# Optimization experiments

Measured on AMD Instinct MI355X. Metric: run time of the kernel, lower is better.

## Reference

```python
import jax, jax.numpy as jnp
import numpy as np

N = 20000      # total nodes (100 graphs x 200 nodes)
B = 100        # batch_size
PER = 200      # nodes per graph (uniform) -> max_num_nodes
E = 320000     # edges (before self-loops)
F_IN = 32      # num_features
HEADS = 10
OUT = 128      # output_dim
NEG_SLOPE = 0.2  # PyG GATConv default


def setup_inputs() -> dict:
    key = jax.random.key(0)
    ks = jax.random.split(key, 14)
    feats = jax.random.normal(ks[0], (N, F_IN), jnp.float32)
    src = jax.random.randint(ks[1], (E,), 0, N)
    dst = jax.random.randint(ks[2], (E,), 0, N)
    edge_index = jnp.stack([src, dst]).astype(jnp.int32)
    graph_id = jnp.repeat(jnp.arange(B, dtype=jnp.int32), PER)
    batch_num_nodes = jnp.full((B,), PER, jnp.int32)
    s1 = 1.0 / np.sqrt(F_IN)
    s2 = 1.0 / np.sqrt(F_IN * HEADS)
    s3 = 1.0 / np.sqrt(OUT)
    return {
        "feats": feats,
        "edge_index": edge_index,
        "graph_id": graph_id,
        "batch_num_nodes": batch_num_nodes,
        # GATConv 1: in F_IN -> HEADS x F_IN, concat
        "W1": jax.random.normal(ks[3], (F_IN, HEADS * F_IN), jnp.float32) * s1,
        "a1_src": jax.random.normal(ks[4], (HEADS, F_IN), jnp.float32) * s1,
        "a1_dst": jax.random.normal(ks[5], (HEADS, F_IN), jnp.float32) * s1,
        "b1": jnp.zeros((HEADS * F_IN,), jnp.float32),
        "W2": jax.random.normal(ks[6], (HEADS * F_IN, OUT), jnp.float32) * s2,
        "a2_src": jax.random.normal(ks[7], (1, OUT), jnp.float32) * s3,
        "a2_dst": jax.random.normal(ks[8], (1, OUT), jnp.float32) * s3,
        "b2": jnp.zeros((OUT,), jnp.float32),
        # shared fc_g1
        "fc_w": jax.random.normal(ks[9], (OUT, OUT), jnp.float32) * s3,
        "fc_b": jnp.zeros((OUT,), jnp.float32),
    }


def gat_conv(x, src, dst, W, a_src, a_dst, bias, heads, out_dim):
    # x: [N, Fin]; src/dst already include self-loops (PyG default add_self_loops=True)
    n = x.shape[0]
    xw = (x @ W).reshape(n, heads, out_dim)                 # [N,H,F]
    s_src = jnp.einsum('nhf,hf->nh', xw, a_src)             # [N,H]
    s_dst = jnp.einsum('nhf,hf->nh', xw, a_dst)
    e = jax.nn.leaky_relu(s_src[src] + s_dst[dst], NEG_SLOPE)  # [E,H]
    # segment softmax over incoming edges of each destination node
    m = jax.ops.segment_max(e, dst, num_segments=n)         # [N,H]
    ex = jnp.exp(e - m[dst])
    denom = jax.ops.segment_sum(ex, dst, num_segments=n)    # [N,H]
    alpha = ex / jnp.maximum(denom[dst], 1e-16)             # [E,H]
    out = jax.ops.segment_sum(alpha[:, :, None] * xw[src], dst, num_segments=n)  # [N,H,F]
    return out.reshape(n, heads * out_dim) + bias


def reference(feats, edge_index, graph_id, batch_num_nodes,
              W1, a1_src, a1_dst, b1, W2, a2_src, a2_dst, b2, fc_w, fc_b):
    n = feats.shape[0]
    loops = jnp.arange(n, dtype=edge_index.dtype)
    src = jnp.concatenate([edge_index[0], loops])
    dst = jnp.concatenate([edge_index[1], loops])
    x = feats.astype(jnp.float32)
    # dropout layers are identity in eval mode
    x = jax.nn.elu(gat_conv(x, src, dst, W1, a1_src, a1_dst, b1, HEADS, F_IN))
    x = gat_conv(x, src, dst, W2, a2_src, a2_dst, b2, 1, OUT)
    x = jax.nn.relu(x)                                       # [N, OUT]
    # dgl_split: scatter node feats into [B, max_num_nodes, OUT] padded tensor
    cum = jnp.concatenate([jnp.zeros((1,), jnp.int32),
                           jnp.cumsum(batch_num_nodes).astype(jnp.int32)])
    idx = jnp.arange(n, dtype=jnp.int32) - cum[graph_id] + graph_id * PER
    padded = jnp.zeros((B * PER, OUT), x.dtype).at[idx].set(x).reshape(B, PER, OUT)
    out = jax.nn.relu(padded @ fc_w + fc_b)                  # [B, PER, OUT]
    # global max pool per graph, then shared fc_g1 + relu
    pooled = jax.ops.segment_max(x, graph_id, num_segments=B)  # [B, OUT]
    pooled = jax.nn.relu(pooled @ fc_w + fc_b)
    return (out, pooled)
```

## Files before the change

kernel.cpp:

```cpp
#include <hip/hip_runtime.h>

#define N_NODES 20000
#define N_EDGES 320000
#define ETOT    (N_EDGES + N_NODES)
#define HEADS   10
#define F_IN    32
#define C1      (HEADS * F_IN)
#define C2      128
#define NB      100
#define PER     200
#define CAP     96
#define HSTRIDE 328
#define X2STRIDE 136

typedef __attribute__((ext_vector_type(8))) short bf16x8;
typedef __attribute__((ext_vector_type(4))) float floatx4;
typedef _Float16 f16;
typedef _Float16 f16x2 __attribute__((ext_vector_type(2)));
typedef _Float16 f16x8 __attribute__((ext_vector_type(8)));

static __device__ __forceinline__ unsigned short f2bf(float f) {
    unsigned int u = __float_as_uint(f);
    unsigned int r = (u + 0x7fffu + ((u >> 16) & 1u)) >> 16;
    return (unsigned short)r;
}

#define SCAT_BLOCKS  ((ETOT + 255) / 256)
#define SCORE_BLOCKS ((N_NODES + 63) / 64)
#define W2P_BLOCKS   ((C1 * C2 + 255) / 256)
#define W1P_BLOCKS   ((HEADS * F_IN * F_IN + 255) / 256)
#define FCP_BLOCKS   ((C2 * C2 + 255) / 256)
#define F16_BLOCKS   ((N_NODES * F_IN / 4 + 255) / 256)
__global__ __launch_bounds__(256) void mega_prep_kernel(
        const int* __restrict__ ei, int* __restrict__ cursor, int* __restrict__ csr_src,
        const float* __restrict__ feats, f16* __restrict__ feats16,
        const float* __restrict__ W1, unsigned short* __restrict__ W1p,
        const float* __restrict__ W2, unsigned short* __restrict__ W2p,
        const float* __restrict__ fcw, f16* __restrict__ FCp,
        const float* __restrict__ a1s, const float* __restrict__ a1d,
        float* __restrict__ s_src, float* __restrict__ s_dst) {
    unsigned int b = blockIdx.x;
    if (b < SCAT_BLOCKS) {
        int e = b * 256 + threadIdx.x;
        if (e >= ETOT) return;
        int s, d;
        if (e < N_EDGES) { s = ei[e]; d = ei[N_EDGES + e]; }
        else             { s = e - N_EDGES; d = s; }
        int pos = atomicAdd(&cursor[d], 1);
        csr_src[(size_t)d * CAP + pos] = s;
        return;
    }
    b -= SCAT_BLOCKS;
    if (b < SCORE_BLOCKS) {
        __shared__ __align__(16) float A[64 * F_IN];
        __shared__ float Ws[C1], Wd[C1];
        int t = threadIdx.x;
        for (int o = t; o < C1; o += 256) {
            int k = o & 31, h = o >> 5;
            float ss = 0.f, dd = 0.f;
#pragma unroll
            for (int f = 0; f < F_IN; f++) {
                float wv = W1[k * C1 + h * 32 + f];
                ss += wv * a1s[h * 32 + f];
                dd += wv * a1d[h * 32 + f];
            }
            Ws[k * HEADS + h] = ss;
            Wd[k * HEADS + h] = dd;
        }
        int n0 = b * 64;
        int nrows = min(64, N_NODES - n0);
        const float4* fs = (const float4*)(feats + (size_t)n0 * F_IN);
        float4* Af = (float4*)A;
        for (int i = t; i < nrows * 8; i += 256) Af[i] = fs[i];
        __syncthreads();
        for (int o = t; o < nrows * HEADS; o += 256) {
            int nl = o / HEADS, h = o - nl * HEADS;
            const float* ar = A + nl * F_IN;
            float ss = 0.f, dd = 0.f;
#pragma unroll
            for (int k = 0; k < F_IN; k++) {
                float av = ar[k];
                ss += av * Ws[k * HEADS + h];
                dd += av * Wd[k * HEADS + h];
            }
            s_src[(size_t)(n0 + nl) * HEADS + h] = ss;
            s_dst[(size_t)(n0 + nl) * HEADS + h] = dd;
        }
        return;
    }
    b -= SCORE_BLOCKS;
    if (b < W2P_BLOCKS) {
        int o = b * 256 + threadIdx.x;
        if (o >= C1 * C2) return;
        int j    = o & 7;
        int lane = (o >> 3) & 63;
        int ct   = (o >> 9) & 7;
        int kb   = o >> 12;
        int k = kb * 32 + (lane >> 4) * 8 + j;
        int n = ct * 16 + (lane & 15);
        W2p[o] = f2bf(W2[k * C2 + n]);
        return;
    }
    b -= W2P_BLOCKS;
    if (b < W1P_BLOCKS) {
        int o = b * 256 + threadIdx.x;
        if (o >= HEADS * F_IN * F_IN) return;
        int j    = o & 7;
        int lane = (o >> 3) & 63;
        int ct   = (o >> 9) & 1;
        int h    = o >> 10;
        int k = (lane >> 4) * 8 + j;
        int f = ct * 16 + (lane & 15);
        W1p[o] = f2bf(W1[k * C1 + h * 32 + f]);
        return;
    }
    b -= W1P_BLOCKS;
    if (b < FCP_BLOCKS) {
        int o = b * 256 + threadIdx.x;
        if (o >= C2 * C2) return;
        int j    = o & 7;
        int lane = (o >> 3) & 63;
        int ct   = (o >> 9) & 7;
        int kb   = o >> 12;
        int k = kb * 32 + (lane >> 4) * 8 + j;
        int n = ct * 16 + (lane & 15);
        FCp[o] = (f16)fcw[k * C2 + n];
        return;
    }
    b -= FCP_BLOCKS;
    {
        int o = b * 256 + threadIdx.x;
        if (o < N_NODES * F_IN / 4) {
            float4 v = ((const float4*)feats)[o];
            f16* d = feats16 + 4 * o;
            d[0] = (f16)v.x; d[1] = (f16)v.y; d[2] = (f16)v.z; d[3] = (f16)v.w;
        }
    }
}

__global__ __launch_bounds__(256) void aggg1_kernel(
        const f16* __restrict__ feats16, const float* __restrict__ s_src,
        const float* __restrict__ s_dst, const int* __restrict__ deg_arr,
        const int* __restrict__ csr_src, unsigned short* __restrict__ gn) {
    __shared__ __align__(4) f16 shP[4][HEADS * 64];
    __shared__ __align__(8) int shS[4][64];
    int wslot = threadIdx.x >> 6;
    int n = blockIdx.x * 4 + wslot;
    int lane = threadIdx.x & 63;
    int k = lane & 31, half = lane >> 5;
    f16* P = shP[wslot];
    int* S = shS[wslot];
    const f16x2 ones = {(f16)1.f, (f16)1.f};

    int beg = n * CAP, deg = deg_arr[n];
    const float* sdp = s_dst + (size_t)n * HEADS;
    float sd[10];
#pragma unroll
    for (int q = 0; q < 5; q++) {
        float2 v = *(const float2*)(sdp + 2 * q);
        sd[2 * q] = v.x; sd[2 * q + 1] = v.y;
    }
    float g[10], la[10];
#pragma unroll
    for (int h = 0; h < 10; h++) { g[h] = 0.f; la[h] = 0.f; }

    for (int c0 = 0; c0 < deg; c0 += 64) {
        int dc = min(deg - c0, 64);
        bool act = lane < dc;
        int s_e = csr_src[beg + c0 + min(lane, dc - 1)];
        const float* ssp = s_src + (size_t)s_e * HEADS;
        float p[10];
#pragma unroll
        for (int q = 0; q < 5; q++) {
            float2 v = *(const float2*)(ssp + 2 * q);
            float e0 = v.x + sd[2 * q];
            float e1 = v.y + sd[2 * q + 1];
            e0 = (e0 >= 0.f) ? e0 : 0.2f * e0;
            e1 = (e1 >= 0.f) ? e1 : 0.2f * e1;
            p[2 * q]     = act ? __expf(e0) : 0.f;
            p[2 * q + 1] = act ? __expf(e1) : 0.f;
        }
        S[lane] = s_e;
#pragma unroll
        for (int h = 0; h < 10; h++) P[h * 64 + lane] = (f16)p[h];
        asm volatile("s_waitcnt lgkmcnt(0)" ::: "memory");

        int dcp = (dc + 3) & ~3;
        for (int i = 0; i < dcp; i += 4) {
            int e0 = i + half * 2;
            int2 ss2 = *(const int2*)&S[e0];
            f16x2 v;
            v.x = feats16[(size_t)ss2.x * F_IN + k];
            v.y = feats16[(size_t)ss2.y * F_IN + k];
#pragma unroll
            for (int h = 0; h < 10; h++) {
                f16x2 pp = *(const f16x2*)&P[h * 64 + e0];
                g[h]  = __builtin_amdgcn_fdot2(pp, v, g[h], false);
                la[h] = __builtin_amdgcn_fdot2(pp, ones, la[h], false);
            }
        }
        asm volatile("s_waitcnt lgkmcnt(0)" ::: "memory");
    }
#pragma unroll
    for (int h = 0; h < 10; h++) {
        g[h]  += __shfl_xor(g[h], 32);
        la[h] += __shfl_xor(la[h], 32);
    }
    if (half == 0) {
        unsigned short* gp = gn + (size_t)n * C1 + k;
#pragma unroll
        for (int h = 0; h < 10; h++)
            gp[h * 32] = f2bf(g[h] / fmaxf(la[h], 1e-16f));
    }
}

__global__ __launch_bounds__(256) void h1gemm2_kernel(
        const unsigned short* __restrict__ gn, const unsigned short* __restrict__ W1p,
        const float* __restrict__ b1, const unsigned short* __restrict__ W2p,
        const float* __restrict__ a_src, const float* __restrict__ a_dst,
        f16* __restrict__ xw2h, float* __restrict__ s_src2, float* __restrict__ s_dst2) {
    __shared__ unsigned short H[2][16 * HSTRIDE];
    __shared__ float redS[2][2][16], redD[2][2][16];
    int waveId = threadIdx.x >> 6;
    int tl = waveId >> 1;
    int w  = waveId & 1;
    int tile = blockIdx.x * 2 + tl;
    int lane = threadIdx.x & 63;
    int quad = lane >> 4, col = lane & 15;
    int row0 = tile * 16;

#pragma unroll
    for (int hh = 0; hh < 5; hh++) {
        int h = w * 5 + hh;
        bf16x8 a = *(const bf16x8*)(gn + (size_t)(row0 + col) * C1 + h * 32 + quad * 8);
        bf16x8 bA = ((const bf16x8*)W1p)[(h * 2 + 0) * 64 + lane];
        bf16x8 bB = ((const bf16x8*)W1p)[(h * 2 + 1) * 64 + lane];
        floatx4 z = {0.f, 0.f, 0.f, 0.f};
        floatx4 c0 = __builtin_amdgcn_mfma_f32_16x16x32_bf16(a, bA, z, 0, 0, 0);
        floatx4 c1 = __builtin_amdgcn_mfma_f32_16x16x32_bf16(a, bB, z, 0, 0, 0);
        float bias0 = b1[h * 32 + col];
        float bias1 = b1[h * 32 + 16 + col];
#pragma unroll
        for (int reg = 0; reg < 4; reg++) {
            int r = quad * 4 + reg;
            float o0 = c0[reg] + bias0;
            float o1 = c1[reg] + bias1;
            o0 = (o0 > 0.f) ? o0 : (__expf(o0) - 1.f);
            o1 = (o1 > 0.f) ? o1 : (__expf(o1) - 1.f);
            H[tl][r * HSTRIDE + h * 32 + col]      = f2bf(o0);
            H[tl][r * HSTRIDE + h * 32 + 16 + col] = f2bf(o1);
        }
    }
    __syncthreads();

    floatx4 acc[4];
#pragma unroll
    for (int c = 0; c < 4; c++) acc[c] = (floatx4){0.f, 0.f, 0.f, 0.f};
    const bf16x8* pb = (const bf16x8*)W2p;
#pragma unroll
    for (int kb = 0; kb < 10; kb++) {
        bf16x8 a = *(const bf16x8*)&H[tl][(lane & 15) * HSTRIDE + kb * 32 + quad * 8];
#pragma unroll
        for (int c = 0; c < 4; c++) {
            bf16x8 b = pb[(kb * 8 + (4 * w + c)) * 64 + lane];
            acc[c] = __builtin_amdgcn_mfma_f32_16x16x32_bf16(a, b, acc[c], 0, 0, 0);
        }
    }
    float asv[4], adv[4];
#pragma unroll
    for (int c = 0; c < 4; c++) {
        asv[c] = a_src[(4 * w + c) * 16 + col];
        adv[c] = a_dst[(4 * w + c) * 16 + col];
    }
#pragma unroll
    for (int reg = 0; reg < 4; reg++) {
        int row = row0 + quad * 4 + reg;
        float vs = 0.f, vd = 0.f;
#pragma unroll
        for (int c = 0; c < 4; c++) {
            float v = acc[c][reg];
            xw2h[(size_t)row * C2 + (4 * w + c) * 16 + col] = (f16)v;
            vs += v * asv[c];
            vd += v * adv[c];
        }
#pragma unroll
        for (int off = 8; off >= 1; off >>= 1) {
            vs += __shfl_xor(vs, off);
            vd += __shfl_xor(vd, off);
        }
        if (col == 0) { redS[tl][w][quad * 4 + reg] = vs; redD[tl][w][quad * 4 + reg] = vd; }
    }
    __syncthreads();
    if (w == 0) {
        if (lane < 16)
            s_src2[row0 + lane] = redS[tl][0][lane] + redS[tl][1][lane];
        else if (lane < 32)
            s_dst2[row0 + lane - 16] = redD[tl][0][lane - 16] + redD[tl][1][lane - 16];
    }
}

__global__ __launch_bounds__(256) void agg2fc_kernel(
        const f16* __restrict__ xw2h, const float* __restrict__ s_src2,
        const float* __restrict__ s_dst2, const int* __restrict__ deg_arr,
        const int* __restrict__ csr_src, const float* __restrict__ b2,
        const f16* __restrict__ FCp, const float* __restrict__ fcb,
        float* __restrict__ out, int* __restrict__ pooledi) {
    __shared__ __align__(8) int2 shE[4][64];
    __shared__ __align__(16) f16 X[16 * X2STRIDE];
    int wslot = threadIdx.x >> 6;
    int lane = threadIdx.x & 63;
    int row0 = blockIdx.x * 16;
    int2* E = shE[wslot];

#pragma unroll
    for (int rep = 0; rep < 4; rep++) {
        int r = wslot * 4 + rep;
        int n = row0 + r;
        int beg = n * CAP, deg = deg_arr[n];
        float sd = s_dst2[n];
        float l = 0.f, a0 = 0.f, a1 = 0.f;

        for (int c0 = 0; c0 < deg; c0 += 64) {
            int dc = min(deg - c0, 64);
            bool act = lane < dc;
            int s_e = csr_src[beg + c0 + min(lane, dc - 1)];
            float e = s_src2[s_e] + sd;
            e = (e >= 0.f) ? e : 0.2f * e;
            float p = act ? __expf(e) : 0.f;
            float su = p;
#pragma unroll
            for (int off = 32; off >= 1; off >>= 1) su += __shfl_xor(su, off);
            l += su;

            E[lane] = make_int2(s_e, __float_as_int(p));
            asm volatile("s_waitcnt lgkmcnt(0)" ::: "memory");

            int dcr = (dc + 3) & ~3;
            for (int i = 0; i < dcr; i += 4) {
                int2 e0 = E[i + 0], e1 = E[i + 1], e2 = E[i + 2], e3 = E[i + 3];
                f16x2 v0 = *(const f16x2*)(xw2h + (size_t)e0.x * C2 + 2 * lane);
                f16x2 v1 = *(const f16x2*)(xw2h + (size_t)e1.x * C2 + 2 * lane);
                f16x2 v2 = *(const f16x2*)(xw2h + (size_t)e2.x * C2 + 2 * lane);
                f16x2 v3 = *(const f16x2*)(xw2h + (size_t)e3.x * C2 + 2 * lane);
                float p0 = __int_as_float(e0.y), p1 = __int_as_float(e1.y);
                float p2 = __int_as_float(e2.y), p3 = __int_as_float(e3.y);
                a0 += p0 * (float)v0.x + p1 * (float)v1.x + p2 * (float)v2.x + p3 * (float)v3.x;
                a1 += p0 * (float)v0.y + p1 * (float)v1.y + p2 * (float)v2.y + p3 * (float)v3.y;
            }
            asm volatile("s_waitcnt lgkmcnt(0)" ::: "memory");
        }

        float linv = 1.f / fmaxf(l, 1e-16f);
        float2 bb = *(const float2*)(b2 + 2 * lane);
        f16x2 o;
        o.x = (f16)fmaxf(a0 * linv + bb.x, 0.f);
        o.y = (f16)fmaxf(a1 * linv + bb.y, 0.f);
        *(f16x2*)&X[r * X2STRIDE + 2 * lane] = o;
    }
    __syncthreads();

    int quad = lane >> 4, col = lane & 15;
    floatx4 acc[2];
    acc[0] = (floatx4){0.f, 0.f, 0.f, 0.f};
    acc[1] = (floatx4){0.f, 0.f, 0.f, 0.f};
    const f16x8* pb = (const f16x8*)FCp;
#pragma unroll
    for (int kb = 0; kb < 4; kb++) {
        f16x8 a = *(const f16x8*)&X[(lane & 15) * X2STRIDE + kb * 32 + quad * 8];
#pragma unroll
        for (int c = 0; c < 2; c++) {
            int ct = wslot * 2 + c;
            f16x8 b = pb[(kb * 8 + ct) * 64 + lane];
            acc[c] = __builtin_amdgcn_mfma_f32_16x16x32_f16(a, b, acc[c], 0, 0, 0);
        }
    }
#pragma unroll
    for (int c = 0; c < 2; c++) {
        int ct = wslot * 2 + c;
        float bias = fcb[ct * 16 + col];
#pragma unroll
        for (int reg = 0; reg < 4; reg++) {
            int row = row0 + quad * 4 + reg;
            out[(size_t)row * C2 + ct * 16 + col] = fmaxf(acc[c][reg] + bias, 0.f);
        }
    }

    if (threadIdx.x < C2) {
        int c = threadIdx.x;
        int gA = row0 / PER;
        int gB = (row0 + 15) / PER;
        float mA = 0.f, mB = 0.f;
#pragma unroll
        for (int r = 0; r < 16; r++) {
            float v = (float)X[r * X2STRIDE + c];
            if ((row0 + r) / PER == gA) mA = fmaxf(mA, v);
            else                        mB = fmaxf(mB, v);
        }
        atomicMax(&pooledi[gA * C2 + c], __float_as_int(mA));
        if (gB != gA) atomicMax(&pooledi[gB * C2 + c], __float_as_int(mB));
    }
}

__global__ void poolfc_kernel(const int* __restrict__ pooledi, const float* __restrict__ fcw,
                              const float* __restrict__ fcb, float* __restrict__ outp) {
    __shared__ float mx[C2];
    int g = blockIdx.x, t = threadIdx.x;
    mx[t] = __int_as_float(pooledi[g * C2 + t]);
    __syncthreads();
    float acc = 0.f;
    for (int k = 0; k < C2; k++) acc += mx[k] * fcw[k * C2 + t];
    outp[g * C2 + t] = fmaxf(acc + fcb[t], 0.f);
}

extern "C" void kernel_launch(void* const* d_in, const int* in_sizes, int n_in,
                              void* d_out, int out_size, void* d_ws, size_t ws_size,
                              hipStream_t stream) {
    const float* feats = (const float*)d_in[0];
    const int*   ei    = (const int*)d_in[1];
    const float* W1  = (const float*)d_in[4];
    const float* a1s = (const float*)d_in[5];
    const float* a1d = (const float*)d_in[6];
    const float* b1  = (const float*)d_in[7];
    const float* W2  = (const float*)d_in[8];
    const float* a2s = (const float*)d_in[9];
    const float* a2d = (const float*)d_in[10];
    const float* b2  = (const float*)d_in[11];
    const float* fcw = (const float*)d_in[12];
    const float* fcb = (const float*)d_in[13];

    float* out_main = (float*)d_out;
    float* out_pool = (float*)d_out + (size_t)N_NODES * C2;

    char* p = (char*)d_ws;
    auto alloc = [&](size_t bytes) {
        char* r = p;
        p += (bytes + 255) & ~(size_t)255;
        return r;
    };
    unsigned short* gn   = (unsigned short*)alloc(sizeof(short) * (size_t)N_NODES * C1);
    unsigned short* W2p  = (unsigned short*)alloc(sizeof(short) * C1 * C2);
    unsigned short* W1p  = (unsigned short*)alloc(sizeof(short) * HEADS * F_IN * F_IN);
    f16*   FCp     = (f16*)alloc(sizeof(f16) * C2 * C2);
    f16*   feats16 = (f16*)alloc(sizeof(f16) * (size_t)N_NODES * F_IN);
    f16*   xw2h    = (f16*)alloc(sizeof(f16) * (size_t)N_NODES * C2);
    float* s1s    = (float*)alloc(sizeof(float) * N_NODES * HEADS);
    float* s1d    = (float*)alloc(sizeof(float) * N_NODES * HEADS);
    float* s2s    = (float*)alloc(sizeof(float) * N_NODES);
    float* s2d    = (float*)alloc(sizeof(float) * N_NODES);
    const int NZ = N_NODES + NB * C2;
    int* zeros   = (int*)alloc(sizeof(int) * NZ);
    int* cursor  = zeros;
    int* pooledi = zeros + N_NODES;
    int* csr_src = (int*)alloc(sizeof(int) * N_NODES * CAP);

    hipMemsetAsync(zeros, 0, sizeof(int) * NZ, stream);

    mega_prep_kernel<<<SCAT_BLOCKS + SCORE_BLOCKS + W2P_BLOCKS + W1P_BLOCKS + FCP_BLOCKS + F16_BLOCKS,
                       256, 0, stream>>>(
        ei, cursor, csr_src, feats, feats16, W1, W1p, W2, W2p, fcw, FCp,
        a1s, a1d, s1s, s1d);

    aggg1_kernel<<<5000, 256, 0, stream>>>(feats16, s1s, s1d, cursor, csr_src, gn);
    h1gemm2_kernel<<<625, 256, 0, stream>>>(gn, W1p, b1, W2p, a2s, a2d, xw2h, s2s, s2d);
    agg2fc_kernel<<<1250, 256, 0, stream>>>(xw2h, s2s, s2d, cursor, csr_src, b2,
                                            FCp, fcb, out_main, pooledi);
    poolfc_kernel<<<NB, C2, 0, stream>>>(pooledi, fcw, fcb, out_pool);
}
```

Baseline: 166.4 us.

## Fuse layer-1 aggregation with W1/ELU and W2 GEMM into one kernel

```diff
diff --git a/kernel.cpp b/kernel.cpp
--- a/kernel.cpp
+++ b/kernel.cpp
@@ -138,101 +138,99 @@
     }
 }
 
-__global__ __launch_bounds__(256) void aggg1_kernel(
+__global__ __launch_bounds__(256) void agg1h1g2_kernel(
         const f16* __restrict__ feats16, const float* __restrict__ s_src,
         const float* __restrict__ s_dst, const int* __restrict__ deg_arr,
-        const int* __restrict__ csr_src, unsigned short* __restrict__ gn) {
-    __shared__ __align__(4) f16 shP[4][HEADS * 64];
-    __shared__ __align__(8) int shS[4][64];
-    int wslot = threadIdx.x >> 6;
-    int n = blockIdx.x * 4 + wslot;
-    int lane = threadIdx.x & 63;
-    int k = lane & 31, half = lane >> 5;
-    f16* P = shP[wslot];
-    int* S = shS[wslot];
-    const f16x2 ones = {(f16)1.f, (f16)1.f};
-
-    int beg = n * CAP, deg = deg_arr[n];
-    const float* sdp = s_dst + (size_t)n * HEADS;
-    float sd[10];
-#pragma unroll
-    for (int q = 0; q < 5; q++) {
-        float2 v = *(const float2*)(sdp + 2 * q);
-        sd[2 * q] = v.x; sd[2 * q + 1] = v.y;
-    }
-    float g[10], la[10];
-#pragma unroll
-    for (int h = 0; h < 10; h++) { g[h] = 0.f; la[h] = 0.f; }
-
-    for (int c0 = 0; c0 < deg; c0 += 64) {
-        int dc = min(deg - c0, 64);
-        bool act = lane < dc;
-        int s_e = csr_src[beg + c0 + min(lane, dc - 1)];
-        const float* ssp = s_src + (size_t)s_e * HEADS;
-        float p[10];
-#pragma unroll
-        for (int q = 0; q < 5; q++) {
-            float2 v = *(const float2*)(ssp + 2 * q);
-            float e0 = v.x + sd[2 * q];
-            float e1 = v.y + sd[2 * q + 1];
-            e0 = (e0 >= 0.f) ? e0 : 0.2f * e0;
-            e1 = (e1 >= 0.f) ? e1 : 0.2f * e1;
-            p[2 * q]     = act ? __expf(e0) : 0.f;
-            p[2 * q + 1] = act ? __expf(e1) : 0.f;
-        }
-        S[lane] = s_e;
-#pragma unroll
-        for (int h = 0; h < 10; h++) P[h * 64 + lane] = (f16)p[h];
-        asm volatile("s_waitcnt lgkmcnt(0)" ::: "memory");
-
-        int dcp = (dc + 3) & ~3;
-        for (int i = 0; i < dcp; i += 4) {
-            int e0 = i + half * 2;
-            int2 ss2 = *(const int2*)&S[e0];
-            f16x2 v;
-            v.x = feats16[(size_t)ss2.x * F_IN + k];
-            v.y = feats16[(size_t)ss2.y * F_IN + k];
-#pragma unroll
-            for (int h = 0; h < 10; h++) {
-                f16x2 pp = *(const f16x2*)&P[h * 64 + e0];
-                g[h]  = __builtin_amdgcn_fdot2(pp, v, g[h], false);
-                la[h] = __builtin_amdgcn_fdot2(pp, ones, la[h], false);
-            }
-        }
-        asm volatile("s_waitcnt lgkmcnt(0)" ::: "memory");
-    }
-#pragma unroll
-    for (int h = 0; h < 10; h++) {
-        g[h]  += __shfl_xor(g[h], 32);
-        la[h] += __shfl_xor(la[h], 32);
-    }
-    if (half == 0) {
-        unsigned short* gp = gn + (size_t)n * C1 + k;
-#pragma unroll
-        for (int h = 0; h < 10; h++)
-            gp[h * 32] = f2bf(g[h] / fmaxf(la[h], 1e-16f));
-    }
-}
-
-__global__ __launch_bounds__(256) void h1gemm2_kernel(
-        const unsigned short* __restrict__ gn, const unsigned short* __restrict__ W1p,
-        const float* __restrict__ b1, const unsigned short* __restrict__ W2p,
+        const int* __restrict__ csr_src,
+        const unsigned short* __restrict__ W1p, const float* __restrict__ b1,
+        const unsigned short* __restrict__ W2p,
         const float* __restrict__ a_src, const float* __restrict__ a_dst,
         f16* __restrict__ xw2h, float* __restrict__ s_src2, float* __restrict__ s_dst2) {
-    __shared__ unsigned short H[2][16 * HSTRIDE];
-    __shared__ float redS[2][2][16], redD[2][2][16];
-    int waveId = threadIdx.x >> 6;
-    int tl = waveId >> 1;
-    int w  = waveId & 1;
-    int tile = blockIdx.x * 2 + tl;
-    int lane = threadIdx.x & 63;
+    union Smem {
+        struct { f16 P[4][HEADS * 64]; int S[4][64]; } p1;
+        unsigned short H[16 * HSTRIDE];
+    };
+    __shared__ __align__(16) Smem u;
+    __shared__ __align__(16) unsigned short G[16 * HSTRIDE];
+    __shared__ float redS[4][16], redD[4][16];
+
+    int wslot = threadIdx.x >> 6;
+    int lane  = threadIdx.x & 63;
+    int k = lane & 31, half = lane >> 5;
+    int row0 = blockIdx.x * 16;
+    f16* P = u.p1.P[wslot];
+    int* S = u.p1.S[wslot];
+    const f16x2 ones = {(f16)1.f, (f16)1.f};
+    const char* fb = (const char*)feats16 + 2 * k;
+
+    for (int rep = 0; rep < 4; rep++) {
+        int r = wslot * 4 + rep;
+        int n = row0 + r;
+        int beg = n * CAP, deg = deg_arr[n];
+        const float* sdp = s_dst + (size_t)n * HEADS;
+        float sd[10];
+#pragma unroll
+        for (int q = 0; q < 5; q++) {
+            float2 v = *(const float2*)(sdp + 2 * q);
+            sd[2 * q] = v.x; sd[2 * q + 1] = v.y;
+        }
+        float g[10], la[10];
+#pragma unroll
+        for (int h = 0; h < 10; h++) { g[h] = 0.f; la[h] = 0.f; }
+
+        for (int c0 = 0; c0 < deg; c0 += 64) {
+            int dc = min(deg - c0, 64);
+            bool act = lane < dc;
+            int s_e = csr_src[beg + c0 + min(lane, dc - 1)];
+            const float* ssp = s_src + (size_t)s_e * HEADS;
+            float p[10];
+#pragma unroll
+            for (int q = 0; q < 5; q++) {
+                float2 v = *(const float2*)(ssp + 2 * q);
+                float e0 = v.x + sd[2 * q];
+                float e1 = v.y + sd[2 * q + 1];
+                e0 = (e0 >= 0.f) ? e0 : 0.2f * e0;
+                e1 = (e1 >= 0.f) ? e1 : 0.2f * e1;
+                p[2 * q]     = act ? __expf(e0) : 0.f;
+                p[2 * q + 1] = act ? __expf(e1) : 0.f;
+            }
+            S[lane] = s_e << 6;
+#pragma unroll
+            for (int h = 0; h < 10; h++) P[h * 64 + lane] = (f16)p[h];
+            asm volatile("s_waitcnt lgkmcnt(0)" ::: "memory");
+
+            int dcp = (dc + 3) & ~3;
+            for (int i = 0; i < dcp; i += 4) {
+                int e0 = i + half * 2;
+                int2 ss2 = *(const int2*)&S[e0];
+                f16x2 v;
+                v.x = *(const f16*)(fb + ss2.x);
+                v.y = *(const f16*)(fb + ss2.y);
+#pragma unroll
+                for (int h = 0; h < 10; h++) {
+                    f16x2 pp = *(const f16x2*)&P[h * 64 + e0];
+                    g[h]  = __builtin_amdgcn_fdot2(pp, v, g[h], false);
+                    la[h] = __builtin_amdgcn_fdot2(pp, ones, la[h], false);
+                }
+            }
+            asm volatile("s_waitcnt lgkmcnt(0)" ::: "memory");
+        }
+#pragma unroll
+        for (int h = 0; h < 10; h++) {
+            g[h]  += __shfl_xor(g[h], 32);
+            la[h] += __shfl_xor(la[h], 32);
+        }
+        if (half == 0) {
+#pragma unroll
+            for (int h = 0; h < 10; h++)
+                G[r * HSTRIDE + h * 32 + k] = f2bf(g[h] / fmaxf(la[h], 1e-16f));
+        }
+    }
+    __syncthreads();
+
     int quad = lane >> 4, col = lane & 15;
-    int row0 = tile * 16;
-
-#pragma unroll
-    for (int hh = 0; hh < 5; hh++) {
-        int h = w * 5 + hh;
-        bf16x8 a = *(const bf16x8*)(gn + (size_t)(row0 + col) * C1 + h * 32 + quad * 8);
+    for (int h = wslot; h < 10; h += 4) {
+        bf16x8 a = *(const bf16x8*)&G[col * HSTRIDE + h * 32 + quad * 8];
         bf16x8 bA = ((const bf16x8*)W1p)[(h * 2 + 0) * 64 + lane];
         bf16x8 bB = ((const bf16x8*)W1p)[(h * 2 + 1) * 64 + lane];
         floatx4 z = {0.f, 0.f, 0.f, 0.f};
@@ -242,44 +240,44 @@
         float bias1 = b1[h * 32 + 16 + col];
 #pragma unroll
         for (int reg = 0; reg < 4; reg++) {
-            int r = quad * 4 + reg;
+            int rr = quad * 4 + reg;
             float o0 = c0[reg] + bias0;
             float o1 = c1[reg] + bias1;
             o0 = (o0 > 0.f) ? o0 : (__expf(o0) - 1.f);
             o1 = (o1 > 0.f) ? o1 : (__expf(o1) - 1.f);
-            H[tl][r * HSTRIDE + h * 32 + col]      = f2bf(o0);
-            H[tl][r * HSTRIDE + h * 32 + 16 + col] = f2bf(o1);
+            u.H[rr * HSTRIDE + h * 32 + col]      = f2bf(o0);
+            u.H[rr * HSTRIDE + h * 32 + 16 + col] = f2bf(o1);
         }
     }
     __syncthreads();
 
-    floatx4 acc[4];
-#pragma unroll
-    for (int c = 0; c < 4; c++) acc[c] = (floatx4){0.f, 0.f, 0.f, 0.f};
+    floatx4 acc[2];
+    acc[0] = (floatx4){0.f, 0.f, 0.f, 0.f};
+    acc[1] = (floatx4){0.f, 0.f, 0.f, 0.f};
     const bf16x8* pb = (const bf16x8*)W2p;
 #pragma unroll
     for (int kb = 0; kb < 10; kb++) {
-        bf16x8 a = *(const bf16x8*)&H[tl][(lane & 15) * HSTRIDE + kb * 32 + quad * 8];
-#pragma unroll
-        for (int c = 0; c < 4; c++) {
-            bf16x8 b = pb[(kb * 8 + (4 * w + c)) * 64 + lane];
+        bf16x8 a = *(const bf16x8*)&u.H[col * HSTRIDE + kb * 32 + quad * 8];
+#pragma unroll
+        for (int c = 0; c < 2; c++) {
+            bf16x8 b = pb[(kb * 8 + (2 * wslot + c)) * 64 + lane];
             acc[c] = __builtin_amdgcn_mfma_f32_16x16x32_bf16(a, b, acc[c], 0, 0, 0);
         }
     }
-    float asv[4], adv[4];
-#pragma unroll
-    for (int c = 0; c < 4; c++) {
-        asv[c] = a_src[(4 * w + c) * 16 + col];
-        adv[c] = a_dst[(4 * w + c) * 16 + col];
+    float asv[2], adv[2];
+#pragma unroll
+    for (int c = 0; c < 2; c++) {
+        asv[c] = a_src[(2 * wslot + c) * 16 + col];
+        adv[c] = a_dst[(2 * wslot + c) * 16 + col];
     }
 #pragma unroll
     for (int reg = 0; reg < 4; reg++) {
         int row = row0 + quad * 4 + reg;
         float vs = 0.f, vd = 0.f;
 #pragma unroll
-        for (int c = 0; c < 4; c++) {
+        for (int c = 0; c < 2; c++) {
             float v = acc[c][reg];
-            xw2h[(size_t)row * C2 + (4 * w + c) * 16 + col] = (f16)v;
+            xw2h[(size_t)row * C2 + (2 * wslot + c) * 16 + col] = (f16)v;
             vs += v * asv[c];
             vd += v * adv[c];
         }
@@ -288,14 +286,16 @@
             vs += __shfl_xor(vs, off);
             vd += __shfl_xor(vd, off);
         }
-        if (col == 0) { redS[tl][w][quad * 4 + reg] = vs; redD[tl][w][quad * 4 + reg] = vd; }
+        if (col == 0) { redS[wslot][quad * 4 + reg] = vs; redD[wslot][quad * 4 + reg] = vd; }
     }
     __syncthreads();
-    if (w == 0) {
+    if (wslot == 0) {
         if (lane < 16)
-            s_src2[row0 + lane] = redS[tl][0][lane] + redS[tl][1][lane];
-        else if (lane < 32)
-            s_dst2[row0 + lane - 16] = redD[tl][0][lane - 16] + redD[tl][1][lane - 16];
+            s_src2[row0 + lane] = redS[0][lane] + redS[1][lane] + redS[2][lane] + redS[3][lane];
+        else if (lane < 32) {
+            int r2 = lane - 16;
+            s_dst2[row0 + r2] = redD[0][r2] + redD[1][r2] + redD[2][r2] + redD[3][r2];
+        }
     }
 }
 
@@ -311,6 +311,7 @@
     int lane = threadIdx.x & 63;
     int row0 = blockIdx.x * 16;
     int2* E = shE[wslot];
+    const char* xb = (const char*)xw2h + 4 * lane;
 
 #pragma unroll
     for (int rep = 0; rep < 4; rep++) {
@@ -332,16 +333,16 @@
             for (int off = 32; off >= 1; off >>= 1) su += __shfl_xor(su, off);
             l += su;
 
-            E[lane] = make_int2(s_e, __float_as_int(p));
+            E[lane] = make_int2(s_e << 8, __float_as_int(p));
             asm volatile("s_waitcnt lgkmcnt(0)" ::: "memory");
 
             int dcr = (dc + 3) & ~3;
             for (int i = 0; i < dcr; i += 4) {
                 int2 e0 = E[i + 0], e1 = E[i + 1], e2 = E[i + 2], e3 = E[i + 3];
-                f16x2 v0 = *(const f16x2*)(xw2h + (size_t)e0.x * C2 + 2 * lane);
-                f16x2 v1 = *(const f16x2*)(xw2h + (size_t)e1.x * C2 + 2 * lane);
-                f16x2 v2 = *(const f16x2*)(xw2h + (size_t)e2.x * C2 + 2 * lane);
-                f16x2 v3 = *(const f16x2*)(xw2h + (size_t)e3.x * C2 + 2 * lane);
+                f16x2 v0 = *(const f16x2*)(xb + e0.x);
+                f16x2 v1 = *(const f16x2*)(xb + e1.x);
+                f16x2 v2 = *(const f16x2*)(xb + e2.x);
+                f16x2 v3 = *(const f16x2*)(xb + e3.x);
                 float p0 = __int_as_float(e0.y), p1 = __int_as_float(e1.y);
                 float p2 = __int_as_float(e2.y), p3 = __int_as_float(e3.y);
                 a0 += p0 * (float)v0.x + p1 * (float)v1.x + p2 * (float)v2.x + p3 * (float)v3.x;
@@ -437,7 +438,6 @@
         p += (bytes + 255) & ~(size_t)255;
         return r;
     };
-    unsigned short* gn   = (unsigned short*)alloc(sizeof(short) * (size_t)N_NODES * C1);
     unsigned short* W2p  = (unsigned short*)alloc(sizeof(short) * C1 * C2);
     unsigned short* W1p  = (unsigned short*)alloc(sizeof(short) * HEADS * F_IN * F_IN);
     f16*   FCp     = (f16*)alloc(sizeof(f16) * C2 * C2);
@@ -460,8 +460,8 @@
         ei, cursor, csr_src, feats, feats16, W1, W1p, W2, W2p, fcw, FCp,
         a1s, a1d, s1s, s1d);
 
-    aggg1_kernel<<<5000, 256, 0, stream>>>(feats16, s1s, s1d, cursor, csr_src, gn);
-    h1gemm2_kernel<<<625, 256, 0, stream>>>(gn, W1p, b1, W2p, a2s, a2d, xw2h, s2s, s2d);
+    agg1h1g2_kernel<<<1250, 256, 0, stream>>>(feats16, s1s, s1d, cursor, csr_src,
+                                              W1p, b1, W2p, a2s, a2d, xw2h, s2s, s2d);
     agg2fc_kernel<<<1250, 256, 0, stream>>>(xw2h, s2s, s2d, cursor, csr_src, b2,
                                             FCp, fcb, out_main, pooledi);
     poolfc_kernel<<<NB, C2, 0, stream>>>(pooledi, fcw, fcb, out_pool);
```

Measured after the change: 162.8 us. 1.02x faster.
